# Kernel tuning notes

Hardware: AMD Instinct MI355X
Metric: run time of the kernel (lower is better)

## Reference

```python
import jax, jax.numpy as jnp
import numpy as np


def setup_inputs() -> dict:
    key = jax.random.key(0)
    ks = jax.random.split(key, 7)
    B, C, H, W = 8, 64, 256, 256
    ld, mem = C // 8, 128
    return {
        "x": jax.random.normal(ks[0], (B, C, H, W), dtype=jnp.float32),
        "w_sub": jax.random.normal(ks[1], (C, ld), dtype=jnp.float32) * (1.0 / np.sqrt(C)),
        "b_sub": jax.random.normal(ks[2], (ld,), dtype=jnp.float32) * 0.01,
        "w_up": jax.random.normal(ks[3], (ld, C), dtype=jnp.float32) * (1.0 / np.sqrt(ld)),
        "b_up": jax.random.normal(ks[4], (C,), dtype=jnp.float32) * 0.01,
        "mb": jax.random.normal(ks[5], (ld, mem), dtype=jnp.float32),
        "mu": jnp.full((1,), 0.5, dtype=jnp.float32),
    }


def reference(x, w_sub, b_sub, w_up, b_up, mb, mu):
    # x: (B, C, H, W). Attention is computed per (batch, width-stripe).
    B, C, H, W = x.shape
    ld = w_sub.shape[1]  # low_dim = C // squeeze_factor
    # (B, C, H, W) -> (B*W, C, H)
    xs = jnp.transpose(x, (0, 3, 1, 2)).reshape(B * W, C, H)
    # AdaptiveAvgPool1d(1) over H -> (B*W, C)
    y = xs.mean(axis=2)
    # subnet: Linear(C -> ld)
    low = y @ w_sub + b_sub  # (B*W, ld)
    # attention over shared memory bank mb (ld, mem); scale = low_dim ** -0.5
    f1 = (low @ mb) * (float(ld) ** -0.5)  # (B*W, mem)
    f = jax.nn.softmax(f1, axis=-1)
    y1 = f @ mb.T  # (B*W, ld)
    # upnet: Linear(ld -> C) + sigmoid gate
    y2 = jax.nn.sigmoid(y1 @ w_up + b_up)  # (B*W, C)
    out = xs * y2[:, :, None] * mu  # broadcast gate over H
    # (B*W, C, H) -> (B, C, H, W)
    return jnp.transpose(out.reshape(B, W, C, H), (0, 2, 3, 1))
```

## Files before the change

kernel.cpp:

```cpp
#include <hip/hip_runtime.h>
#include <hip/hip_bf16.h>
#include <cstddef>

constexpr int B = 8, C = 64, H = 256, W = 256, LD = 8, MEM = 128;
constexpr int W4 = W / 4;
constexpr int NSTRIPE = B * W;
constexpr int ROWS = 32;

__global__ __launch_bounds__(256) void k_mean(const float* __restrict__ x,
                                              float* __restrict__ ymean) {
    const int bc = blockIdx.x;
    const int b  = bc >> 6;
    const int c  = bc & 63;
    const int t  = threadIdx.x;
    const int w4 = t & 63;
    const int hg = t >> 6;

    const float4* plane = reinterpret_cast<const float4*>(x + (size_t)bc * H * W);
    float sx = 0.f, sy = 0.f, sz = 0.f, sw = 0.f;
    #pragma unroll 4
    for (int h = hg; h < H; h += 4) {
        float4 v = plane[h * W4 + w4];
        sx += v.x; sy += v.y; sz += v.z; sw += v.w;
    }

    __shared__ float4 part[256];
    part[t] = make_float4(sx, sy, sz, sw);
    __syncthreads();

    if (hg == 0) {
        float4 a = part[t], p1 = part[t + 64], p2 = part[t + 128], p3 = part[t + 192];
        const float inv = 1.0f / (float)H;
        float r0 = (a.x + p1.x + p2.x + p3.x) * inv;
        float r1 = (a.y + p1.y + p2.y + p3.y) * inv;
        float r2 = (a.z + p1.z + p2.z + p3.z) * inv;
        float r3 = (a.w + p1.w + p2.w + p3.w) * inv;
        const int wbase = w4 * 4;
        size_t o = ((size_t)b * W + wbase) * C + c;
        ymean[o]         = r0;
        ymean[o + C]     = r1;
        ymean[o + 2 * C] = r2;
        ymean[o + 3 * C] = r3;
    }
}

__global__ __launch_bounds__(128) void k_gate(const float* __restrict__ ymean,
                                              const float* __restrict__ w_sub,
                                              const float* __restrict__ b_sub,
                                              const float* __restrict__ w_up,
                                              const float* __restrict__ b_up,
                                              const float* __restrict__ mb,
                                              const float* __restrict__ mu,
                                              float* __restrict__ gate) {
    const int s = blockIdx.x;
    const int t = threadIdx.x;

    __shared__ float y[C];
    __shared__ float low[LD];
    __shared__ float f[MEM];
    __shared__ float red[MEM];
    __shared__ float y1[LD];

    if (t < C) y[t] = ymean[(size_t)s * C + t];
    __syncthreads();

    if (t < LD) {
        float acc = b_sub[t];
        for (int c = 0; c < C; ++c) acc += y[c] * w_sub[c * LD + t];
        low[t] = acc;
    }
    __syncthreads();

    const float scale = 0.35355339059327373f;
    float v = 0.f;
    #pragma unroll
    for (int l = 0; l < LD; ++l) v += low[l] * mb[l * MEM + t];
    v *= scale;

    red[t] = v;
    __syncthreads();
    for (int off = 64; off > 0; off >>= 1) {
        if (t < off) red[t] = fmaxf(red[t], red[t + off]);
        __syncthreads();
    }
    const float m = red[0];
    __syncthreads();
    const float e = expf(v - m);
    red[t] = e;
    __syncthreads();
    for (int off = 64; off > 0; off >>= 1) {
        if (t < off) red[t] += red[t + off];
        __syncthreads();
    }
    const float invsum = 1.0f / red[0];
    f[t] = e * invsum;
    __syncthreads();

    if (t < LD) {
        float acc = 0.f;
        for (int k = 0; k < MEM; ++k) acc += f[k] * mb[t * MEM + k];
        y1[t] = acc;
    }
    __syncthreads();

    if (t < C) {
        float acc = b_up[t];
        #pragma unroll
        for (int l = 0; l < LD; ++l) acc += y1[l] * w_up[l * C + t];
        float g = 1.0f / (1.0f + expf(-acc));
        gate[(size_t)s * C + t] = g * mu[0];
    }
}

__global__ __launch_bounds__(256) void k_scale(const float* __restrict__ x,
                                               const float* __restrict__ gate,
                                               float* __restrict__ out) {
    const int bc = blockIdx.y;
    const int b  = bc >> 6;
    const int c  = bc & 63;
    const int t  = threadIdx.x;

    __shared__ float g[W];
    if (t < W) g[t] = gate[((size_t)b * W + t) * C + c];
    __syncthreads();

    const int w4 = t & 63;
    const float g0 = g[w4 * 4 + 0];
    const float g1 = g[w4 * 4 + 1];
    const float g2 = g[w4 * 4 + 2];
    const float g3 = g[w4 * 4 + 3];

    const float4* xp = reinterpret_cast<const float4*>(x + (size_t)bc * H * W);
    float4* op       = reinterpret_cast<float4*>(out + (size_t)bc * H * W);

    const int base = blockIdx.x * (ROWS * W4);
    #pragma unroll 4
    for (int i = t; i < ROWS * W4; i += 256) {
        const int idx = base + i;
        float4 v = xp[idx];
        v.x *= g0; v.y *= g1; v.z *= g2; v.w *= g3;
        op[idx] = v;
    }
}

extern "C" void kernel_launch(void* const* d_in, const int* in_sizes, int n_in,
                              void* d_out, int out_size, void* d_ws, size_t ws_size,
                              hipStream_t stream) {
    const float* x     = (const float*)d_in[0];
    const float* w_sub = (const float*)d_in[1];
    const float* b_sub = (const float*)d_in[2];
    const float* w_up  = (const float*)d_in[3];
    const float* b_up  = (const float*)d_in[4];
    const float* mb    = (const float*)d_in[5];
    const float* mu    = (const float*)d_in[6];
    float* out = (float*)d_out;

    float* ymean = (float*)d_ws;
    float* gate  = ymean + (size_t)NSTRIPE * C;

    k_mean<<<B * C, 256, 0, stream>>>(x, ymean);
    k_gate<<<NSTRIPE, 128, 0, stream>>>(ymean, w_sub, b_sub, w_up, b_up, mb, mu, gate);
    k_scale<<<dim3(H / ROWS, B * C), 256, 0, stream>>>(x, gate, out);
}
```

Measured before the change: 268.7 us.

## Split mean reduction over H quarters, parallelize gate math, transpose gate layout

The mean kernel now launches four blocks per (batch, channel) plane, each summing a quarter of H and writing partial sums. The gate kernel then combines these partials. The gate kernel's serial per-thread dot products and shared-memory tree reductions are replaced with wave shuffle reductions spread across all 128 threads. Gates are stored transposed (channel-major), so the scale kernel reads them contiguously and pulls them as one float4. This raises parallelism in the reduction and cuts serial latency in the small gate kernel, at the cost of extra partial-sum traffic.

```diff
diff --git a/kernel.cpp b/kernel.cpp
--- a/kernel.cpp
+++ b/kernel.cpp
@@ -5,115 +5,138 @@
 constexpr int B = 8, C = 64, H = 256, W = 256, LD = 8, MEM = 128;
 constexpr int W4 = W / 4;
 constexpr int NSTRIPE = B * W;
+constexpr int NQ = 4;
 constexpr int ROWS = 32;
 
-__global__ __launch_bounds__(256) void k_mean(const float* __restrict__ x,
-                                              float* __restrict__ ymean) {
-    const int bc = blockIdx.x;
-    const int b  = bc >> 6;
-    const int c  = bc & 63;
+__global__ __launch_bounds__(256) void k_mean_part(const float* __restrict__ x,
+                                                   float4* __restrict__ part4) {
+    const int gb = blockIdx.x;
+    const int bc = gb >> 2;
+    const int q  = gb & 3;
     const int t  = threadIdx.x;
     const int w4 = t & 63;
     const int hg = t >> 6;
 
     const float4* plane = reinterpret_cast<const float4*>(x + (size_t)bc * H * W);
     float sx = 0.f, sy = 0.f, sz = 0.f, sw = 0.f;
-    #pragma unroll 4
-    for (int h = hg; h < H; h += 4) {
-        float4 v = plane[h * W4 + w4];
+    const int h0 = q * 64 + hg;
+    #pragma unroll
+    for (int i = 0; i < 16; ++i) {
+        float4 v = plane[(h0 + i * 4) * W4 + w4];
         sx += v.x; sy += v.y; sz += v.z; sw += v.w;
     }
 
-    __shared__ float4 part[256];
-    part[t] = make_float4(sx, sy, sz, sw);
+    __shared__ float4 red[256];
+    red[t] = make_float4(sx, sy, sz, sw);
     __syncthreads();
 
     if (hg == 0) {
-        float4 a = part[t], p1 = part[t + 64], p2 = part[t + 128], p3 = part[t + 192];
-        const float inv = 1.0f / (float)H;
-        float r0 = (a.x + p1.x + p2.x + p3.x) * inv;
-        float r1 = (a.y + p1.y + p2.y + p3.y) * inv;
-        float r2 = (a.z + p1.z + p2.z + p3.z) * inv;
-        float r3 = (a.w + p1.w + p2.w + p3.w) * inv;
-        const int wbase = w4 * 4;
-        size_t o = ((size_t)b * W + wbase) * C + c;
-        ymean[o]         = r0;
-        ymean[o + C]     = r1;
-        ymean[o + 2 * C] = r2;
-        ymean[o + 3 * C] = r3;
+        float4 a = red[t], p1 = red[t + 64], p2 = red[t + 128], p3 = red[t + 192];
+        float4 r;
+        r.x = a.x + p1.x + p2.x + p3.x;
+        r.y = a.y + p1.y + p2.y + p3.y;
+        r.z = a.z + p1.z + p2.z + p3.z;
+        r.w = a.w + p1.w + p2.w + p3.w;
+        part4[(size_t)gb * W4 + w4] = r;
     }
 }
 
-__global__ __launch_bounds__(128) void k_gate(const float* __restrict__ ymean,
+__global__ __launch_bounds__(128) void k_gate(const float* __restrict__ part,
                                               const float* __restrict__ w_sub,
                                               const float* __restrict__ b_sub,
                                               const float* __restrict__ w_up,
                                               const float* __restrict__ b_up,
                                               const float* __restrict__ mb,
                                               const float* __restrict__ mu,
-                                              float* __restrict__ gate) {
+                                              float* __restrict__ gateT) {
     const int s = blockIdx.x;
+    const int b = s >> 8;
+    const int w = s & 255;
     const int t = threadIdx.x;
 
     __shared__ float y[C];
     __shared__ float low[LD];
     __shared__ float f[MEM];
-    __shared__ float red[MEM];
+    __shared__ float wred[4];
     __shared__ float y1[LD];
+    __shared__ float red2[128];
 
-    if (t < C) y[t] = ymean[(size_t)s * C + t];
-    __syncthreads();
+    {
+        const int c  = t & 63;
+        const int qh = t >> 6;
+        const float* pc = part + (((size_t)(b * C + c) * NQ + qh * 2) * W + w);
+        red2[t] = pc[0] + pc[W];
+        __syncthreads();
+        if (t < C) y[t] = (red2[t] + red2[t + 64]) * (1.0f / (float)H);
+        __syncthreads();
+    }
 
-    if (t < LD) {
-        float acc = b_sub[t];
-        for (int c = 0; c < C; ++c) acc += y[c] * w_sub[c * LD + t];
-        low[t] = acc;
+    const int l = t >> 4;
+    const int i = t & 15;
+
+    {
+        float acc = 0.f;
+        #pragma unroll
+        for (int j = 0; j < 4; ++j) {
+            const int c = i + 16 * j;
+            acc += y[c] * w_sub[c * LD + l];
+        }
+        acc += __shfl_xor(acc, 1);
+        acc += __shfl_xor(acc, 2);
+        acc += __shfl_xor(acc, 4);
+        acc += __shfl_xor(acc, 8);
+        if (i == 0) low[l] = acc + b_sub[l];
     }
     __syncthreads();
 
-    const float scale = 0.35355339059327373f;
     float v = 0.f;
     #pragma unroll
-    for (int l = 0; l < LD; ++l) v += low[l] * mb[l * MEM + t];
-    v *= scale;
+    for (int ll = 0; ll < LD; ++ll) v += low[ll] * mb[ll * MEM + t];
+    v *= 0.35355339059327373f;
 
-    red[t] = v;
+    float m = v;
+    #pragma unroll
+    for (int mask = 1; mask <= 32; mask <<= 1) m = fmaxf(m, __shfl_xor(m, mask));
+    const int wid = t >> 6;
+    if ((t & 63) == 0) wred[wid] = m;
     __syncthreads();
-    for (int off = 64; off > 0; off >>= 1) {
-        if (t < off) red[t] = fmaxf(red[t], red[t + off]);
-        __syncthreads();
-    }
-    const float m = red[0];
+    m = fmaxf(wred[0], wred[1]);
+
+    const float e = expf(v - m);
+    f[t] = e;
+    float sm = e;
+    #pragma unroll
+    for (int mask = 1; mask <= 32; mask <<= 1) sm += __shfl_xor(sm, mask);
+    if ((t & 63) == 0) wred[2 + wid] = sm;
     __syncthreads();
-    const float e = expf(v - m);
-    red[t] = e;
-    __syncthreads();
-    for (int off = 64; off > 0; off >>= 1) {
-        if (t < off) red[t] += red[t + off];
-        __syncthreads();
-    }
-    const float invsum = 1.0f / red[0];
-    f[t] = e * invsum;
-    __syncthreads();
+    const float invsum = 1.0f / (wred[2] + wred[3]);
 
-    if (t < LD) {
+    {
         float acc = 0.f;
-        for (int k = 0; k < MEM; ++k) acc += f[k] * mb[t * MEM + k];
-        y1[t] = acc;
+        #pragma unroll
+        for (int j = 0; j < 8; ++j) {
+            const int k = i * 8 + j;
+            acc += f[k] * mb[l * MEM + k];
+        }
+        acc += __shfl_xor(acc, 1);
+        acc += __shfl_xor(acc, 2);
+        acc += __shfl_xor(acc, 4);
+        acc += __shfl_xor(acc, 8);
+        if (i == 0) y1[l] = acc * invsum;
     }
     __syncthreads();
 
     if (t < C) {
         float acc = b_up[t];
         #pragma unroll
-        for (int l = 0; l < LD; ++l) acc += y1[l] * w_up[l * C + t];
-        float g = 1.0f / (1.0f + expf(-acc));
-        gate[(size_t)s * C + t] = g * mu[0];
+        for (int ll = 0; ll < LD; ++ll) acc += y1[ll] * w_up[ll * C + t];
+        const float g = mu[0] / (1.0f + expf(-acc));
+        gateT[(size_t)t * NSTRIPE + s] = g;
     }
 }
 
 __global__ __launch_bounds__(256) void k_scale(const float* __restrict__ x,
-                                               const float* __restrict__ gate,
+                                               const float* __restrict__ gateT,
                                                float* __restrict__ out) {
     const int bc = blockIdx.y;
     const int b  = bc >> 6;
@@ -121,24 +144,20 @@
     const int t  = threadIdx.x;
 
     __shared__ float g[W];
-    if (t < W) g[t] = gate[((size_t)b * W + t) * C + c];
+    g[t] = gateT[(size_t)c * NSTRIPE + b * W + t];
     __syncthreads();
 
     const int w4 = t & 63;
-    const float g0 = g[w4 * 4 + 0];
-    const float g1 = g[w4 * 4 + 1];
-    const float g2 = g[w4 * 4 + 2];
-    const float g3 = g[w4 * 4 + 3];
+    const float4 gv = reinterpret_cast<const float4*>(g)[w4];
 
     const float4* xp = reinterpret_cast<const float4*>(x + (size_t)bc * H * W);
     float4* op       = reinterpret_cast<float4*>(out + (size_t)bc * H * W);
 
     const int base = blockIdx.x * (ROWS * W4);
-    #pragma unroll 4
-    for (int i = t; i < ROWS * W4; i += 256) {
-        const int idx = base + i;
+    #pragma unroll 8
+    for (int idx = base + t; idx < base + ROWS * W4; idx += 256) {
         float4 v = xp[idx];
-        v.x *= g0; v.y *= g1; v.z *= g2; v.w *= g3;
+        v.x *= gv.x; v.y *= gv.y; v.z *= gv.z; v.w *= gv.w;
         op[idx] = v;
     }
 }
@@ -155,10 +174,10 @@
     const float* mu    = (const float*)d_in[6];
     float* out = (float*)d_out;
 
-    float* ymean = (float*)d_ws;
-    float* gate  = ymean + (size_t)NSTRIPE * C;
+    float* part  = (float*)d_ws;
+    float* gateT = part + (size_t)B * C * NQ * W;
 
-    k_mean<<<B * C, 256, 0, stream>>>(x, ymean);
-    k_gate<<<NSTRIPE, 128, 0, stream>>>(ymean, w_sub, b_sub, w_up, b_up, mb, mu, gate);
-    k_scale<<<dim3(H / ROWS, B * C), 256, 0, stream>>>(x, gate, out);
+    k_mean_part<<<B * C * NQ, 256, 0, stream>>>(x, (float4*)part);
+    k_gate<<<NSTRIPE, 128, 0, stream>>>(part, w_sub, b_sub, w_up, b_up, mb, mu, gateT);
+    k_scale<<<dim3(H / ROWS, B * C), 256, 0, stream>>>(x, gateT, out);
 }
```

Result: no change. 271.5 us (+1.0%).
